# Kernel tuning notes

Measured on AMD Instinct MI355X. Metric: run time of the kernel, lower is better.

## Reference

```python
import jax, jax.numpy as jnp
import numpy as np

B = 16384      # batch of protein embeddings
C = 128        # n_channels
F = 5000       # number of GO terms (functions)
E_CHILD = 15000  # parent->child edges (~3 children per term)


def setup_inputs() -> dict:
    key = jax.random.key(0)
    k_x, k_w, k_p, k_c = jax.random.split(key, 4)
    x = jax.random.normal(k_x, (B, C), dtype=jnp.float32)
    W = jax.random.normal(k_w, (C, F), dtype=jnp.float32) * 0.05
    b = jnp.zeros((F,), dtype=jnp.float32)
    # random GO DAG edges; every node also gets a self-edge so the max
    # aggregation covers {self} U children, exactly like the torch loop
    parents = jax.random.randint(k_p, (E_CHILD,), 0, F, dtype=jnp.int32)
    childs = jax.random.randint(k_c, (E_CHILD,), 0, F, dtype=jnp.int32)
    self_idx = jnp.arange(F, dtype=jnp.int32)
    edge_parent = jnp.concatenate([self_idx, parents])  # [20000]
    edge_child = jnp.concatenate([self_idx, childs])    # [20000]
    return {"x": x, "W": W, "b": b,
            "edge_parent": edge_parent, "edge_child": edge_child}


def reference(x, W, b, edge_parent, edge_child):
    # Fused version of the 5000 separate Linear(C,1)+Sigmoid heads
    probs = jax.nn.sigmoid(x @ W + b)          # [B, F]
    # Hierarchical max over {self} U children via segment-max on edge list
    vals = probs.T[edge_child]                  # [E, B]
    agg = jax.ops.segment_max(vals, edge_parent, num_segments=F)  # [F, B]
    return agg.T                                # [B, F]
```

## Files before the change

### kernel.cpp

```cpp
#include <hip/hip_runtime.h>
#include <hip/hip_bf16.h>

#define BDIM 16384
#define CDIM 128
#define FDIM 5000
#define EDIM 20000
#define ELLW 16
#define MAXOVF 20000
#define NT4  10

typedef __attribute__((ext_vector_type(8))) short short8;
typedef __attribute__((ext_vector_type(4))) float f32x4;
typedef __attribute__((ext_vector_type(2))) float f32x2;
typedef __attribute__((ext_vector_type(2))) int i32x2;
typedef __attribute__((ext_vector_type(8))) unsigned short upk8;
typedef __attribute__((ext_vector_type(4))) unsigned short upk4;
typedef __attribute__((ext_vector_type(2))) unsigned short upk2;
typedef __attribute__((ext_vector_type(2))) unsigned int u32x2;
typedef __attribute__((ext_vector_type(4))) unsigned int u32x4;

__device__ __forceinline__ unsigned short f2bf(float f) {
    unsigned int u = __builtin_bit_cast(unsigned int, f);
    u = (u + 0x7fffu + ((u >> 16) & 1u)) >> 16;
    return (unsigned short)u;
}
__device__ __forceinline__ unsigned int pkmax2(unsigned int a, unsigned int b) {
#if __has_builtin(__builtin_elementwise_max)
    upk2 r = __builtin_elementwise_max(__builtin_bit_cast(upk2, a),
                                       __builtin_bit_cast(upk2, b));
    return __builtin_bit_cast(unsigned int, r);
#else
    unsigned int lo = ((a & 0xFFFFu) > (b & 0xFFFFu)) ? (a & 0xFFFFu) : (b & 0xFFFFu);
    unsigned int hi = ((a >> 16) > (b >> 16)) ? (a & 0xFFFF0000u) : (b & 0xFFFF0000u);
    return lo | hi;
#endif
}
__device__ __forceinline__ unsigned int lo16x2(unsigned int v) {
#if __has_builtin(__builtin_amdgcn_perm)
    return __builtin_amdgcn_perm(0u, v, 0x0C010C00u);
#else
    return (v & 0xFFu) | ((v << 8) & 0x00FF0000u);
#endif
}
__device__ __forceinline__ unsigned int hi16x2(unsigned int v) {
#if __has_builtin(__builtin_amdgcn_perm)
    return __builtin_amdgcn_perm(0u, v, 0x0C030C02u);
#else
    return ((v >> 16) & 0xFFu) | ((v >> 8) & 0x00FF0000u);
#endif
}
__device__ __forceinline__ float fast_rcp(float x) {
#if __has_builtin(__builtin_amdgcn_rcpf)
    return __builtin_amdgcn_rcpf(x);
#else
    return 1.0f / x;
#endif
}
__device__ __forceinline__ void gll16(const unsigned short* g, unsigned short* l) {
    __builtin_amdgcn_global_load_lds(
        (const __attribute__((address_space(1))) void*)g,
        (__attribute__((address_space(3))) void*)l, 16, 0, 0);
}

__global__ __launch_bounds__(256) void prep1_kernel(
    const float* __restrict__ x, const float* __restrict__ W,
    unsigned short* __restrict__ xb, unsigned short* __restrict__ wt,
    unsigned short* __restrict__ ell, int* __restrict__ cur,
    int* __restrict__ ovf_cnt)
{
    __shared__ float lt[128][33];
    int bid = blockIdx.x, tid = threadIdx.x;
    if (bid < 1024) {
        size_t base = (size_t)bid * 2048 + (size_t)tid * 8;
        const f32x4* p = (const f32x4*)(x + base);
        f32x4 v0 = p[0], v1 = p[1];
        short8 o;
        o[0] = (short)f2bf(v0[0]); o[1] = (short)f2bf(v0[1]);
        o[2] = (short)f2bf(v0[2]); o[3] = (short)f2bf(v0[3]);
        o[4] = (short)f2bf(v1[0]); o[5] = (short)f2bf(v1[1]);
        o[6] = (short)f2bf(v1[2]); o[7] = (short)f2bf(v1[3]);
        *(short8*)(xb + base) = o;
    } else if (bid < 1181) {
        int f0 = (bid - 1024) * 32;
        int f_l = tid & 31, k0 = (tid >> 5) * 16;
        #pragma unroll
        for (int i = 0; i < 16; ++i) {
            int f = f0 + f_l;
            lt[k0 + i][f_l] = (f < FDIM) ? W[(size_t)(k0 + i) * FDIM + f] : 0.f;
        }
        __syncthreads();
        int f_l2 = tid >> 3, ks = (tid & 7) * 16;
        int f = f0 + f_l2;
        if (f < FDIM) {
            short8 o0, o1;
            #pragma unroll
            for (int j = 0; j < 8; ++j) o0[j] = (short)f2bf(lt[ks + j][f_l2]);
            #pragma unroll
            for (int j = 0; j < 8; ++j) o1[j] = (short)f2bf(lt[ks + 8 + j][f_l2]);
            *(short8*)(wt + (size_t)f * 128 + ks)     = o0;
            *(short8*)(wt + (size_t)f * 128 + ks + 8) = o1;
        }
    } else {
        int p = (bid - 1181) * 256 + tid;
        if (p < FDIM) {
            upk8 s;
            #pragma unroll
            for (int j = 0; j < 8; ++j) s[j] = (unsigned short)p;
            *(upk8*)(ell + (size_t)p * ELLW)     = s;
            *(upk8*)(ell + (size_t)p * ELLW + 8) = s;
            cur[p] = 1;
        }
        if (p == FDIM) *ovf_cnt = 0;
    }
}

__global__ __launch_bounds__(256) void prep2_kernel(
    const int* __restrict__ epar, const int* __restrict__ echild,
    int* __restrict__ cur, unsigned short* __restrict__ ell,
    int* __restrict__ ovf_cnt, int* __restrict__ ovf_pairs)
{
    int i = blockIdx.x * 256 + threadIdx.x;
    if (i < EDIM) {
        int p = epar[i], c = echild[i];
        if (p != c) {
            int pos = atomicAdd(&cur[p], 1);
            if (pos < ELLW) {
                ell[(size_t)p * ELLW + pos] = (unsigned short)c;
            } else {
                int j = atomicAdd(ovf_cnt, 1);
                if (j < MAXOVF) { ovf_pairs[2 * j] = p; ovf_pairs[2 * j + 1] = c; }
            }
        }
    }
}

__global__ __launch_bounds__(1024) void prep3_kernel(
    const int* __restrict__ cur, const unsigned short* __restrict__ ell,
    unsigned int* __restrict__ dgp, unsigned short* __restrict__ ellp)
{
    __shared__ int hist[32];
    __shared__ int base[32];
    int tid = threadIdx.x;
    if (tid < 32) hist[tid] = 0;
    __syncthreads();
    for (int p = tid; p < FDIM; p += 1024) {
        int d = cur[p]; if (d > 31) d = 31;
        atomicAdd(&hist[d], 1);
    }
    __syncthreads();
    if (tid == 0) {
        int acc = 0;
        for (int b = 0; b < 32; ++b) { base[b] = acc; acc += hist[b]; }
    }
    __syncthreads();
    for (int p = tid; p < FDIM; p += 1024) {
        int d = cur[p]; if (d > 31) d = 31;
        int pos = atomicAdd(&base[d], 1);
        int dcap = cur[p]; if (dcap > 255) dcap = 255;
        dgp[pos] = ((unsigned int)p << 8) | (unsigned int)dcap;
    }
    __syncthreads();
    for (int i = tid; i < FDIM; i += 1024) {
        int pr = (int)(dgp[i] >> 8);
        upk8 lo = *(const upk8*)(ell + (size_t)pr * ELLW);
        upk8 hi = *(const upk8*)(ell + (size_t)pr * ELLW + 8);
        *(upk8*)(ellp + (size_t)i * ELLW)     = lo;
        *(upk8*)(ellp + (size_t)i * ELLW + 8) = hi;
    }
}

__global__ __launch_bounds__(512, 4) void gemm8u_kernel(
    const unsigned short* __restrict__ xb,
    const unsigned short* __restrict__ wt,
    const float* __restrict__ bias,
    unsigned char* __restrict__ probs8)
{
    __shared__ unsigned short lA[128 * 128];
    __shared__ unsigned short lB[128 * 128];

    int bid0 = blockIdx.x;
    int bid  = (bid0 & 7) * (128 * NT4 / 8) + (bid0 >> 3);
    int bm = bid / NT4, bq = bid % NT4;
    int tid = threadIdx.x;
    int lane = tid & 63, w = tid >> 6;
    int wm = w >> 2, wn = w & 3;
    int g = lane >> 4, lr = lane & 15;
    int lrow = lane >> 4;
    int lcol = (lane & 15) << 4;

    auto stageA = [&]() {
        #pragma unroll
        for (int it = 0; it < 4; ++it) {
            int ci = w * 4 + it;
            int row = ci * 4 + lrow;
            int sw = lcol ^ ((row & 7) << 4);
            gll16(xb + ((size_t)(bm * 128 + row) << 7) + (sw >> 1),
                  lA + ci * 512);
        }
    };
    auto stageB = [&](int bn) {
        #pragma unroll
        for (int it = 0; it < 4; ++it) {
            int ci = w * 4 + it;
            int row = ci * 4 + lrow;
            int sw = lcol ^ ((row & 7) << 4);
            gll16(wt + ((size_t)(bn * 128 + row) << 7) + (sw >> 1),
                  lB + ci * 512);
        }
    };
    auto compute = [&](f32x4 (&acc)[4][2]) {
        #pragma unroll
        for (int ks = 0; ks < 4; ++ks) {
            int cbk = ks * 64 + g * 16;
            short8 af[4], bf[2];
            #pragma unroll
            for (int mi = 0; mi < 4; ++mi) {
                int row = wm * 64 + mi * 16 + lr;
                af[mi] = *(const short8*)((const char*)lA + row * 256 + (cbk ^ ((row & 7) << 4)));
            }
            #pragma unroll
            for (int nj = 0; nj < 2; ++nj) {
                int row = wn * 32 + nj * 16 + lr;
                bf[nj] = *(const short8*)((const char*)lB + row * 256 + (cbk ^ ((row & 7) << 4)));
            }
            #pragma unroll
            for (int mi = 0; mi < 4; ++mi)
                #pragma unroll
                for (int nj = 0; nj < 2; ++nj)
                    acc[mi][nj] = __builtin_amdgcn_mfma_f32_16x16x32_bf16(
                        af[mi], bf[nj], acc[mi][nj], 0, 0, 0);
        }
    };
    auto epilogue = [&](int bn, f32x4 (&acc)[4][2]) {
        #pragma unroll
        for (int nj = 0; nj < 2; ++nj) {
            int f = bn * 128 + wn * 32 + nj * 16 + lr;
            bool ok = (f < FDIM);
            float bb = ok ? bias[f] : 0.f;
            #pragma unroll
            for (int mi = 0; mi < 4; ++mi) {
                unsigned int pk = 0;
                #pragma unroll
                for (int j = 0; j < 4; ++j) {
                    float z = acc[mi][nj][j] + bb;
                    float pr = fast_rcp(1.0f + __expf(-z));
                    unsigned int q = (unsigned int)(pr * 255.f + 0.5f);
                    pk |= q << (8 * j);
                }
                if (ok) {
                    int slab = bm * 16 + wm * 8 + mi * 2 + (g >> 1);
                    int grp  = slab * 2 + (g & 1);
                    *(unsigned int*)(probs8 + ((size_t)grp * FDIM + f) * 4) = pk;
                }
            }
        }
    };

    stageA();
    stageB(bq * 4);
    __syncthreads();

    f32x4 zero = {0.f, 0.f, 0.f, 0.f};
    for (int t = 0; t < 4; ++t) {
        f32x4 acc[4][2];
        #pragma unroll
        for (int mi = 0; mi < 4; ++mi) { acc[mi][0] = zero; acc[mi][1] = zero; }
        compute(acc);
        if (t < 3) {
            __syncthreads();
            stageB(bq * 4 + t + 1);
            epilogue(bq * 4 + t, acc);
            __syncthreads();
        } else {
            epilogue(bq * 4 + t, acc);
        }
    }
}

__global__ __launch_bounds__(1024) void segmax19c_kernel(
    const unsigned char* __restrict__ probs8,
    const unsigned int* __restrict__ dgp,
    const unsigned short* __restrict__ ellp,
    const int* __restrict__ ovf_cnt, const int* __restrict__ ovf_pairs,
    float* __restrict__ out)
{
    __shared__ unsigned int l32[FDIM];
    __shared__ unsigned int xlo[FDIM];
    __shared__ unsigned int xhi[FDIM];
    int grp = blockIdx.x;
    int b0 = (grp >> 1) * 8 + (grp & 1) * 4;
    int tid = threadIdx.x;
    const unsigned short* src =
        (const unsigned short*)(probs8 + (size_t)grp * FDIM * 4);

    for (int c = tid; c < FDIM / 4; c += 1024) {
        gll16(src + (size_t)c * 8, (unsigned short*)l32 + (size_t)c * 8);
    }
    __syncthreads();

    int novf = *ovf_cnt; if (novf > MAXOVF) novf = MAXOVF;

    for (int w0 = tid * 2; w0 < FDIM; w0 += 2048) {
        int w1 = w0 + 1;
        u32x2 dv = *(const u32x2*)(dgp + w0);
        int pa = (int)(dv[0] >> 8), da = (int)(dv[0] & 255u);
        int pb = (int)(dv[1] >> 8), db = (int)(dv[1] & 255u);
        upk8 ea = *(const upk8*)(ellp + (size_t)w0 * ELLW);
        upk8 eb = *(const upk8*)(ellp + (size_t)w1 * ELLW);
        unsigned int va = l32[ea[0]], vb = l32[eb[0]];
        unsigned int alo = lo16x2(va), ahi = hi16x2(va);
        unsigned int blo = lo16x2(vb), bhi = hi16x2(vb);
        #pragma unroll
        for (int s = 1; s < 4; ++s) {
            unsigned int u = l32[ea[s]], v = l32[eb[s]];
            alo = pkmax2(alo, lo16x2(u)); ahi = pkmax2(ahi, hi16x2(u));
            blo = pkmax2(blo, lo16x2(v)); bhi = pkmax2(bhi, hi16x2(v));
        }
        if (da > 4) {
            #pragma unroll
            for (int s = 4; s < 8; ++s) {
                unsigned int u = l32[ea[s]];
                alo = pkmax2(alo, lo16x2(u)); ahi = pkmax2(ahi, hi16x2(u));
            }
        }
        if (db > 4) {
            #pragma unroll
            for (int s = 4; s < 8; ++s) {
                unsigned int v = l32[eb[s]];
                blo = pkmax2(blo, lo16x2(v)); bhi = pkmax2(bhi, hi16x2(v));
            }
        }
        if (da > 8) {
            upk8 e = *(const upk8*)(ellp + (size_t)w0 * ELLW + 8);
            #pragma unroll
            for (int k = 0; k < 8; ++k) {
                unsigned int u = l32[e[k]];
                alo = pkmax2(alo, lo16x2(u)); ahi = pkmax2(ahi, hi16x2(u));
            }
        }
        if (db > 8) {
            upk8 e = *(const upk8*)(ellp + (size_t)w1 * ELLW + 8);
            #pragma unroll
            for (int k = 0; k < 8; ++k) {
                unsigned int v = l32[e[k]];
                blo = pkmax2(blo, lo16x2(v)); bhi = pkmax2(bhi, hi16x2(v));
            }
        }
        if (da > ELLW) {
            for (int i = 0; i < novf; ++i)
                if (ovf_pairs[2 * i] == pa) {
                    unsigned int u = l32[ovf_pairs[2 * i + 1]];
                    alo = pkmax2(alo, lo16x2(u)); ahi = pkmax2(ahi, hi16x2(u));
                }
        }
        if (db > ELLW) {
            for (int i = 0; i < novf; ++i)
                if (ovf_pairs[2 * i] == pb) {
                    unsigned int v = l32[ovf_pairs[2 * i + 1]];
                    blo = pkmax2(blo, lo16x2(v)); bhi = pkmax2(bhi, hi16x2(v));
                }
        }
        xlo[pa] = alo; xhi[pa] = ahi;
        xlo[pb] = blo; xhi[pb] = bhi;
    }
    __syncthreads();

    for (int p0 = tid * 4; p0 < FDIM; p0 += 4096) {
        u32x4 lo4 = *(const u32x4*)(xlo + p0);
        u32x4 hi4 = *(const u32x4*)(xhi + p0);
        size_t o = (size_t)b0 * FDIM + p0;
        #pragma unroll
        for (int r = 0; r < 4; ++r) {
            f32x4 v4;
            #pragma unroll
            for (int j = 0; j < 4; ++j) {
                unsigned int w = (r < 2) ? lo4[j] : hi4[j];
                unsigned int q = (w >> (16 * (r & 1))) & 0xFFFFu;
                v4[j] = (float)q * (1.f / 255.f);
            }
            *(f32x4*)(out + o + (size_t)r * FDIM) = v4;
        }
    }
}

extern "C" void kernel_launch(void* const* d_in, const int* in_sizes, int n_in,
                              void* d_out, int out_size, void* d_ws, size_t ws_size,
                              hipStream_t stream)
{
    const float* x     = (const float*)d_in[0];
    const float* W     = (const float*)d_in[1];
    const float* bias  = (const float*)d_in[2];
    const int*   epar  = (const int*)d_in[3];
    const int*   echild= (const int*)d_in[4];
    float* out = (float*)d_out;

    char* ws = (char*)d_ws;
    size_t off = 0;
    auto alloc = [&](size_t bytes) { size_t o = off; off = (off + bytes + 255) & ~(size_t)255; return o; };
    size_t o_probs  = alloc((size_t)BDIM * FDIM);
    size_t o_xb     = alloc((size_t)BDIM * CDIM * 2);
    size_t o_wt     = alloc((size_t)FDIM * CDIM * 2);
    size_t o_ell    = alloc((size_t)FDIM * ELLW * 2);
    size_t o_cur    = alloc((size_t)FDIM * 4);
    size_t o_ovfc   = alloc(4);
    size_t o_ovfp   = alloc((size_t)MAXOVF * 8);
    size_t o_dgp    = alloc((size_t)FDIM * 4);
    size_t o_ellp   = alloc((size_t)FDIM * ELLW * 2);
    (void)ws_size; (void)in_sizes; (void)n_in; (void)out_size;

    unsigned char*  probs8 = (unsigned char*)(ws + o_probs);
    unsigned short* xb     = (unsigned short*)(ws + o_xb);
    unsigned short* wt     = (unsigned short*)(ws + o_wt);
    unsigned short* ell    = (unsigned short*)(ws + o_ell);
    int* cur      = (int*)(ws + o_cur);
    int* ovf_cnt  = (int*)(ws + o_ovfc);
    int* ovf_pairs= (int*)(ws + o_ovfp);
    unsigned int*   dgp  = (unsigned int*)(ws + o_dgp);
    unsigned short* ellp = (unsigned short*)(ws + o_ellp);

    prep1_kernel<<<1201, 256, 0, stream>>>(x, W, xb, wt, ell, cur, ovf_cnt);
    prep2_kernel<<<79, 256, 0, stream>>>(epar, echild, cur, ell, ovf_cnt, ovf_pairs);
    prep3_kernel<<<1, 1024, 0, stream>>>(cur, ell, dgp, ellp);
    gemm8u_kernel<<<128 * NT4, 512, 0, stream>>>(xb, wt, bias, probs8);
    segmax19c_kernel<<<BDIM / 8 * 2, 1024, 0, stream>>>(probs8, dgp, ellp,
                                                        ovf_cnt, ovf_pairs, out);
}
```

Measured before the change: 144.2 us.

## Drop degree-sorting prep kernel and fuse segment-max gather with output write

Removes the single-block prep3 kernel that bucketed parents by degree and permuted the ELL table. The segment-max kernel now walks parents in natural order, four per thread, reading degrees from cur and children from the unpermuted ELL. Results are written straight to global output, so the shared-memory xlo/xhi staging buffers and one barrier are gone. This saves a serial launch and cuts LDS use, which may raise occupancy, but loses degree-sorted warp uniformity and so adds branch divergence in the gather loop.

```diff
diff --git a/kernel.cpp b/kernel.cpp
--- a/kernel.cpp
+++ b/kernel.cpp
@@ -13,6 +13,7 @@
 typedef __attribute__((ext_vector_type(4))) float f32x4;
 typedef __attribute__((ext_vector_type(2))) float f32x2;
 typedef __attribute__((ext_vector_type(2))) int i32x2;
+typedef __attribute__((ext_vector_type(4))) int i32x4;
 typedef __attribute__((ext_vector_type(8))) unsigned short upk8;
 typedef __attribute__((ext_vector_type(4))) unsigned short upk4;
 typedef __attribute__((ext_vector_type(2))) unsigned short upk2;
@@ -134,41 +135,6 @@
     }
 }
 
-__global__ __launch_bounds__(1024) void prep3_kernel(
-    const int* __restrict__ cur, const unsigned short* __restrict__ ell,
-    unsigned int* __restrict__ dgp, unsigned short* __restrict__ ellp)
-{
-    __shared__ int hist[32];
-    __shared__ int base[32];
-    int tid = threadIdx.x;
-    if (tid < 32) hist[tid] = 0;
-    __syncthreads();
-    for (int p = tid; p < FDIM; p += 1024) {
-        int d = cur[p]; if (d > 31) d = 31;
-        atomicAdd(&hist[d], 1);
-    }
-    __syncthreads();
-    if (tid == 0) {
-        int acc = 0;
-        for (int b = 0; b < 32; ++b) { base[b] = acc; acc += hist[b]; }
-    }
-    __syncthreads();
-    for (int p = tid; p < FDIM; p += 1024) {
-        int d = cur[p]; if (d > 31) d = 31;
-        int pos = atomicAdd(&base[d], 1);
-        int dcap = cur[p]; if (dcap > 255) dcap = 255;
-        dgp[pos] = ((unsigned int)p << 8) | (unsigned int)dcap;
-    }
-    __syncthreads();
-    for (int i = tid; i < FDIM; i += 1024) {
-        int pr = (int)(dgp[i] >> 8);
-        upk8 lo = *(const upk8*)(ell + (size_t)pr * ELLW);
-        upk8 hi = *(const upk8*)(ell + (size_t)pr * ELLW + 8);
-        *(upk8*)(ellp + (size_t)i * ELLW)     = lo;
-        *(upk8*)(ellp + (size_t)i * ELLW + 8) = hi;
-    }
-}
-
 __global__ __launch_bounds__(512, 4) void gemm8u_kernel(
     const unsigned short* __restrict__ xb,
     const unsigned short* __restrict__ wt,
@@ -277,16 +243,13 @@
     }
 }
 
-__global__ __launch_bounds__(1024) void segmax19c_kernel(
+__global__ __launch_bounds__(1024) void segmax21_kernel(
     const unsigned char* __restrict__ probs8,
-    const unsigned int* __restrict__ dgp,
-    const unsigned short* __restrict__ ellp,
+    const int* __restrict__ cur, const unsigned short* __restrict__ ell,
     const int* __restrict__ ovf_cnt, const int* __restrict__ ovf_pairs,
     float* __restrict__ out)
 {
     __shared__ unsigned int l32[FDIM];
-    __shared__ unsigned int xlo[FDIM];
-    __shared__ unsigned int xhi[FDIM];
     int grp = blockIdx.x;
     int b0 = (grp >> 1) * 8 + (grp & 1) * 4;
     int tid = threadIdx.x;
@@ -300,81 +263,51 @@
 
     int novf = *ovf_cnt; if (novf > MAXOVF) novf = MAXOVF;
 
-    for (int w0 = tid * 2; w0 < FDIM; w0 += 2048) {
-        int w1 = w0 + 1;
-        u32x2 dv = *(const u32x2*)(dgp + w0);
-        int pa = (int)(dv[0] >> 8), da = (int)(dv[0] & 255u);
-        int pb = (int)(dv[1] >> 8), db = (int)(dv[1] & 255u);
-        upk8 ea = *(const upk8*)(ellp + (size_t)w0 * ELLW);
-        upk8 eb = *(const upk8*)(ellp + (size_t)w1 * ELLW);
-        unsigned int va = l32[ea[0]], vb = l32[eb[0]];
-        unsigned int alo = lo16x2(va), ahi = hi16x2(va);
-        unsigned int blo = lo16x2(vb), bhi = hi16x2(vb);
-        #pragma unroll
-        for (int s = 1; s < 4; ++s) {
-            unsigned int u = l32[ea[s]], v = l32[eb[s]];
-            alo = pkmax2(alo, lo16x2(u)); ahi = pkmax2(ahi, hi16x2(u));
-            blo = pkmax2(blo, lo16x2(v)); bhi = pkmax2(bhi, hi16x2(v));
-        }
-        if (da > 4) {
-            #pragma unroll
-            for (int s = 4; s < 8; ++s) {
-                unsigned int u = l32[ea[s]];
-                alo = pkmax2(alo, lo16x2(u)); ahi = pkmax2(ahi, hi16x2(u));
-            }
-        }
-        if (db > 4) {
-            #pragma unroll
-            for (int s = 4; s < 8; ++s) {
-                unsigned int v = l32[eb[s]];
-                blo = pkmax2(blo, lo16x2(v)); bhi = pkmax2(bhi, hi16x2(v));
-            }
-        }
-        if (da > 8) {
-            upk8 e = *(const upk8*)(ellp + (size_t)w0 * ELLW + 8);
-            #pragma unroll
-            for (int k = 0; k < 8; ++k) {
-                unsigned int u = l32[e[k]];
-                alo = pkmax2(alo, lo16x2(u)); ahi = pkmax2(ahi, hi16x2(u));
-            }
-        }
-        if (db > 8) {
-            upk8 e = *(const upk8*)(ellp + (size_t)w1 * ELLW + 8);
-            #pragma unroll
-            for (int k = 0; k < 8; ++k) {
-                unsigned int v = l32[e[k]];
-                blo = pkmax2(blo, lo16x2(v)); bhi = pkmax2(bhi, hi16x2(v));
-            }
-        }
-        if (da > ELLW) {
-            for (int i = 0; i < novf; ++i)
-                if (ovf_pairs[2 * i] == pa) {
-                    unsigned int u = l32[ovf_pairs[2 * i + 1]];
-                    alo = pkmax2(alo, lo16x2(u)); ahi = pkmax2(ahi, hi16x2(u));
+    for (int p0 = tid * 4; p0 < FDIM; p0 += 4096) {
+        i32x4 dg4 = *(const i32x4*)(cur + p0);
+        unsigned int alo[4], ahi[4];
+        #pragma unroll
+        for (int j = 0; j < 4; ++j) {
+            int p = p0 + j;
+            upk8 e = *(const upk8*)(ell + (size_t)p * ELLW);
+            unsigned int v = l32[e[0]];
+            unsigned int lo = lo16x2(v), hi = hi16x2(v);
+            #pragma unroll
+            for (int s = 1; s < 4; ++s) {
+                unsigned int u = l32[e[s]];
+                lo = pkmax2(lo, lo16x2(u)); hi = pkmax2(hi, hi16x2(u));
+            }
+            if (dg4[j] > 4) {
+                #pragma unroll
+                for (int s = 4; s < 8; ++s) {
+                    unsigned int u = l32[e[s]];
+                    lo = pkmax2(lo, lo16x2(u)); hi = pkmax2(hi, hi16x2(u));
                 }
-        }
-        if (db > ELLW) {
-            for (int i = 0; i < novf; ++i)
-                if (ovf_pairs[2 * i] == pb) {
-                    unsigned int v = l32[ovf_pairs[2 * i + 1]];
-                    blo = pkmax2(blo, lo16x2(v)); bhi = pkmax2(bhi, hi16x2(v));
+            }
+            if (dg4[j] > 8) {
+                upk8 e2 = *(const upk8*)(ell + (size_t)p * ELLW + 8);
+                #pragma unroll
+                for (int k = 0; k < 8; ++k) {
+                    unsigned int u = l32[e2[k]];
+                    lo = pkmax2(lo, lo16x2(u)); hi = pkmax2(hi, hi16x2(u));
                 }
-        }
-        xlo[pa] = alo; xhi[pa] = ahi;
-        xlo[pb] = blo; xhi[pb] = bhi;
-    }
-    __syncthreads();
-
-    for (int p0 = tid * 4; p0 < FDIM; p0 += 4096) {
-        u32x4 lo4 = *(const u32x4*)(xlo + p0);
-        u32x4 hi4 = *(const u32x4*)(xhi + p0);
+            }
+            if (dg4[j] > ELLW) {
+                for (int i = 0; i < novf; ++i)
+                    if (ovf_pairs[2 * i] == p) {
+                        unsigned int u = l32[ovf_pairs[2 * i + 1]];
+                        lo = pkmax2(lo, lo16x2(u)); hi = pkmax2(hi, hi16x2(u));
+                    }
+            }
+            alo[j] = lo; ahi[j] = hi;
+        }
         size_t o = (size_t)b0 * FDIM + p0;
         #pragma unroll
         for (int r = 0; r < 4; ++r) {
             f32x4 v4;
             #pragma unroll
             for (int j = 0; j < 4; ++j) {
-                unsigned int w = (r < 2) ? lo4[j] : hi4[j];
+                unsigned int w = (r < 2) ? alo[j] : ahi[j];
                 unsigned int q = (w >> (16 * (r & 1))) & 0xFFFFu;
                 v4[j] = (float)q * (1.f / 255.f);
             }
@@ -404,8 +337,6 @@
     size_t o_cur    = alloc((size_t)FDIM * 4);
     size_t o_ovfc   = alloc(4);
     size_t o_ovfp   = alloc((size_t)MAXOVF * 8);
-    size_t o_dgp    = alloc((size_t)FDIM * 4);
-    size_t o_ellp   = alloc((size_t)FDIM * ELLW * 2);
     (void)ws_size; (void)in_sizes; (void)n_in; (void)out_size;
 
     unsigned char*  probs8 = (unsigned char*)(ws + o_probs);
@@ -415,13 +346,10 @@
     int* cur      = (int*)(ws + o_cur);
     int* ovf_cnt  = (int*)(ws + o_ovfc);
     int* ovf_pairs= (int*)(ws + o_ovfp);
-    unsigned int*   dgp  = (unsigned int*)(ws + o_dgp);
-    unsigned short* ellp = (unsigned short*)(ws + o_ellp);
 
     prep1_kernel<<<1201, 256, 0, stream>>>(x, W, xb, wt, ell, cur, ovf_cnt);
     prep2_kernel<<<79, 256, 0, stream>>>(epar, echild, cur, ell, ovf_cnt, ovf_pairs);
-    prep3_kernel<<<1, 1024, 0, stream>>>(cur, ell, dgp, ellp);
     gemm8u_kernel<<<128 * NT4, 512, 0, stream>>>(xb, wt, bias, probs8);
-    segmax19c_kernel<<<BDIM / 8 * 2, 1024, 0, stream>>>(probs8, dgp, ellp,
-                                                        ovf_cnt, ovf_pairs, out);
-}
+    segmax21_kernel<<<BDIM / 8 * 2, 1024, 0, stream>>>(probs8, cur, ell,
+                                                       ovf_cnt, ovf_pairs, out);
+}
```

Measured after the change: 174.5 us. 21.0% more time.

## Fold edge scatter into GEMM launch and drop permuted ELL copy

Applied to the files above, without the earlier changes.

The separate edge-scatter kernel becomes 40 extra blocks at the front of the GEMM grid, and the permutation step that built a degree-sorted copy of the ELL table is removed. The segmax kernel now indexes the original ELL table through the parent id stored in dgp, and prep3 only builds the sorted degree list after the GEMM. This cuts one launch and one small serial kernel from the chain. In exchange, the ELL reads in segmax become scattered rather than contiguous, and the scatter blocks now share the GPU with the GEMM blocks.

```diff
diff --git a/kernel.cpp b/kernel.cpp
--- a/kernel.cpp
+++ b/kernel.cpp
@@ -8,6 +8,8 @@
 #define ELLW 16
 #define MAXOVF 20000
 #define NT4  10
+#define NGEMM (128 * NT4)
+#define NP2   40
 
 typedef __attribute__((ext_vector_type(8))) short short8;
 typedef __attribute__((ext_vector_type(4))) float f32x4;
@@ -114,29 +116,8 @@
     }
 }
 
-__global__ __launch_bounds__(256) void prep2_kernel(
-    const int* __restrict__ epar, const int* __restrict__ echild,
-    int* __restrict__ cur, unsigned short* __restrict__ ell,
-    int* __restrict__ ovf_cnt, int* __restrict__ ovf_pairs)
-{
-    int i = blockIdx.x * 256 + threadIdx.x;
-    if (i < EDIM) {
-        int p = epar[i], c = echild[i];
-        if (p != c) {
-            int pos = atomicAdd(&cur[p], 1);
-            if (pos < ELLW) {
-                ell[(size_t)p * ELLW + pos] = (unsigned short)c;
-            } else {
-                int j = atomicAdd(ovf_cnt, 1);
-                if (j < MAXOVF) { ovf_pairs[2 * j] = p; ovf_pairs[2 * j + 1] = c; }
-            }
-        }
-    }
-}
-
-__global__ __launch_bounds__(1024) void prep3_kernel(
-    const int* __restrict__ cur, const unsigned short* __restrict__ ell,
-    unsigned int* __restrict__ dgp, unsigned short* __restrict__ ellp)
+__global__ __launch_bounds__(1024) void prep3lite_kernel(
+    const int* __restrict__ cur, unsigned int* __restrict__ dgp)
 {
     __shared__ int hist[32];
     __shared__ int base[32];
@@ -159,29 +140,43 @@
         int dcap = cur[p]; if (dcap > 255) dcap = 255;
         dgp[pos] = ((unsigned int)p << 8) | (unsigned int)dcap;
     }
-    __syncthreads();
-    for (int i = tid; i < FDIM; i += 1024) {
-        int pr = (int)(dgp[i] >> 8);
-        upk8 lo = *(const upk8*)(ell + (size_t)pr * ELLW);
-        upk8 hi = *(const upk8*)(ell + (size_t)pr * ELLW + 8);
-        *(upk8*)(ellp + (size_t)i * ELLW)     = lo;
-        *(upk8*)(ellp + (size_t)i * ELLW + 8) = hi;
-    }
-}
-
-__global__ __launch_bounds__(512, 4) void gemm8u_kernel(
+}
+
+__global__ __launch_bounds__(512, 4) void gemm8u2_kernel(
     const unsigned short* __restrict__ xb,
     const unsigned short* __restrict__ wt,
     const float* __restrict__ bias,
-    unsigned char* __restrict__ probs8)
+    unsigned char* __restrict__ probs8,
+    const int* __restrict__ epar, const int* __restrict__ echild,
+    int* __restrict__ cur, unsigned short* __restrict__ ell,
+    int* __restrict__ ovf_cnt, int* __restrict__ ovf_pairs)
 {
     __shared__ unsigned short lA[128 * 128];
     __shared__ unsigned short lB[128 * 128];
 
     int bid0 = blockIdx.x;
-    int bid  = (bid0 & 7) * (128 * NT4 / 8) + (bid0 >> 3);
+    int tid = threadIdx.x;
+
+    if (bid0 < NP2) {
+        int i = bid0 * 512 + tid;
+        if (i < EDIM) {
+            int p = epar[i], c = echild[i];
+            if (p != c) {
+                int pos = atomicAdd(&cur[p], 1);
+                if (pos < ELLW) {
+                    ell[(size_t)p * ELLW + pos] = (unsigned short)c;
+                } else {
+                    int j = atomicAdd(ovf_cnt, 1);
+                    if (j < MAXOVF) { ovf_pairs[2 * j] = p; ovf_pairs[2 * j + 1] = c; }
+                }
+            }
+        }
+        return;
+    }
+
+    int bg   = bid0 - NP2;
+    int bid  = (bg & 7) * (NGEMM / 8) + (bg >> 3);
     int bm = bid / NT4, bq = bid % NT4;
-    int tid = threadIdx.x;
     int lane = tid & 63, w = tid >> 6;
     int wm = w >> 2, wn = w & 3;
     int g = lane >> 4, lr = lane & 15;
@@ -277,10 +272,10 @@
     }
 }
 
-__global__ __launch_bounds__(1024) void segmax19c_kernel(
+__global__ __launch_bounds__(1024) void segmax19d_kernel(
     const unsigned char* __restrict__ probs8,
     const unsigned int* __restrict__ dgp,
-    const unsigned short* __restrict__ ellp,
+    const unsigned short* __restrict__ ell,
     const int* __restrict__ ovf_cnt, const int* __restrict__ ovf_pairs,
     float* __restrict__ out)
 {
@@ -305,8 +300,8 @@
         u32x2 dv = *(const u32x2*)(dgp + w0);
         int pa = (int)(dv[0] >> 8), da = (int)(dv[0] & 255u);
         int pb = (int)(dv[1] >> 8), db = (int)(dv[1] & 255u);
-        upk8 ea = *(const upk8*)(ellp + (size_t)w0 * ELLW);
-        upk8 eb = *(const upk8*)(ellp + (size_t)w1 * ELLW);
+        upk8 ea = *(const upk8*)(ell + (size_t)pa * ELLW);
+        upk8 eb = *(const upk8*)(ell + (size_t)pb * ELLW);
         unsigned int va = l32[ea[0]], vb = l32[eb[0]];
         unsigned int alo = lo16x2(va), ahi = hi16x2(va);
         unsigned int blo = lo16x2(vb), bhi = hi16x2(vb);
@@ -331,7 +326,7 @@
             }
         }
         if (da > 8) {
-            upk8 e = *(const upk8*)(ellp + (size_t)w0 * ELLW + 8);
+            upk8 e = *(const upk8*)(ell + (size_t)pa * ELLW + 8);
             #pragma unroll
             for (int k = 0; k < 8; ++k) {
                 unsigned int u = l32[e[k]];
@@ -339,7 +334,7 @@
             }
         }
         if (db > 8) {
-            upk8 e = *(const upk8*)(ellp + (size_t)w1 * ELLW + 8);
+            upk8 e = *(const upk8*)(ell + (size_t)pb * ELLW + 8);
             #pragma unroll
             for (int k = 0; k < 8; ++k) {
                 unsigned int v = l32[e[k]];
@@ -405,7 +400,6 @@
     size_t o_ovfc   = alloc(4);
     size_t o_ovfp   = alloc((size_t)MAXOVF * 8);
     size_t o_dgp    = alloc((size_t)FDIM * 4);
-    size_t o_ellp   = alloc((size_t)FDIM * ELLW * 2);
     (void)ws_size; (void)in_sizes; (void)n_in; (void)out_size;
 
     unsigned char*  probs8 = (unsigned char*)(ws + o_probs);
@@ -415,13 +409,13 @@
     int* cur      = (int*)(ws + o_cur);
     int* ovf_cnt  = (int*)(ws + o_ovfc);
     int* ovf_pairs= (int*)(ws + o_ovfp);
-    unsigned int*   dgp  = (unsigned int*)(ws + o_dgp);
-    unsigned short* ellp = (unsigned short*)(ws + o_ellp);
+    unsigned int* dgp = (unsigned int*)(ws + o_dgp);
 
     prep1_kernel<<<1201, 256, 0, stream>>>(x, W, xb, wt, ell, cur, ovf_cnt);
-    prep2_kernel<<<79, 256, 0, stream>>>(epar, echild, cur, ell, ovf_cnt, ovf_pairs);
-    prep3_kernel<<<1, 1024, 0, stream>>>(cur, ell, dgp, ellp);
-    gemm8u_kernel<<<128 * NT4, 512, 0, stream>>>(xb, wt, bias, probs8);
-    segmax19c_kernel<<<BDIM / 8 * 2, 1024, 0, stream>>>(probs8, dgp, ellp,
+    gemm8u2_kernel<<<NP2 + NGEMM, 512, 0, stream>>>(xb, wt, bias, probs8,
+                                                    epar, echild, cur, ell,
+                                                    ovf_cnt, ovf_pairs);
+    prep3lite_kernel<<<1, 1024, 0, stream>>>(cur, dgp);
+    segmax19d_kernel<<<BDIM / 8 * 2, 1024, 0, stream>>>(probs8, dgp, ell,
                                                         ovf_cnt, ovf_pairs, out);
 }
```

Result: slower. 160.5 us (+11.3%).
